# Kernel optimization log

Hardware: AMD Instinct MI355X
Metric: run time of the kernel (lower is better)

## Reference

```python
import jax, jax.numpy as jnp
import numpy as np

N_NODES = 50000
N_EDGES = 800000
D_IN = 256
D_HID = 256
D_OUT = 256


def setup_inputs() -> dict:
    key = jax.random.key(0)
    ks = jax.random.split(key, 14)
    s = 1.0 / np.sqrt(D_IN)
    inp = {
        "x": jax.random.normal(ks[0], (N_NODES, D_IN), dtype=jnp.float32),
        "edge_index": jax.random.randint(ks[1], (2, N_EDGES), 0, N_NODES, dtype=jnp.int64),
        "edge_attr": jax.random.uniform(ks[2], (N_EDGES, 1), dtype=jnp.float32),
        # GCNConv layer weights (3 layers)
        "W1": jax.random.normal(ks[3], (D_IN, D_HID), dtype=jnp.float32) * s,
        "b1": jnp.zeros((D_HID,), dtype=jnp.float32),
        "W2": jax.random.normal(ks[4], (D_HID, D_HID), dtype=jnp.float32) * s,
        "b2": jnp.zeros((D_HID,), dtype=jnp.float32),
        "W3": jax.random.normal(ks[5], (D_HID, D_OUT), dtype=jnp.float32) * s,
        "b3": jnp.zeros((D_OUT,), dtype=jnp.float32),
        # edge MLP: Linear(1,8) -> ReLU -> Linear(8,1) -> Sigmoid
        "mw1": jax.random.normal(ks[6], (1, 8), dtype=jnp.float32),
        "mb1": jnp.zeros((8,), dtype=jnp.float32),
        "mw2": jax.random.normal(ks[7], (8, 1), dtype=jnp.float32) * (1.0 / np.sqrt(8.0)),
        "mb2": jnp.zeros((1,), dtype=jnp.float32),
    }
    return inp


def _gcn_layer(x, src, dst, ew, W, b, n):
    """PyG GCNConv: add self-loops (weight 1), symmetric normalization."""
    deg = jax.ops.segment_sum(ew, dst, num_segments=n) + 1.0  # self-loop contributes 1
    dinv = jax.lax.rsqrt(deg)                                 # [N]
    norm = dinv[src] * ew * dinv[dst]                         # [E]
    h = x @ W + b                                             # [N, d_out]
    agg = jax.ops.segment_sum(h[src] * norm[:, None], dst, num_segments=n)
    # self-loop term: dinv[i] * 1 * dinv[i] = 1/deg[i]
    return agg + h * (1.0 / deg)[:, None]


def reference(x, edge_index, edge_attr, W1, b1, W2, b2, W3, b3, mw1, mb1, mw2, mb2):
    src, dst = edge_index[0], edge_index[1]
    # edge weight MLP with sigmoid gate
    h = jax.nn.relu(edge_attr @ mw1 + mb1)
    ew = jax.nn.sigmoid(h @ mw2 + mb2)[:, 0]  # [E]

    n = x.shape[0]
    x = jax.nn.relu(_gcn_layer(x, src, dst, ew, W1, b1, n))  # dropout inactive (eval)
    x = jax.nn.relu(_gcn_layer(x, src, dst, ew, W2, b2, n))
    x = _gcn_layer(x, src, dst, ew, W3, b3, n)
    return x
```

## Files before the change

### kernel.cpp

```cpp
#include <hip/hip_runtime.h>
#include <hip/hip_bf16.h>
#include <stdint.h>

#define GCN_N 50000
#define GCN_E 800000
#define GCN_D 256

typedef __attribute__((ext_vector_type(8))) short bf16x8;
typedef __attribute__((ext_vector_type(4))) float f32x4;
typedef unsigned short ushort_t;
typedef unsigned long long u64;

__device__ __forceinline__ float bf2f(ushort_t u) {
    return __uint_as_float(((unsigned)u) << 16);
}
__device__ __forceinline__ ushort_t f2bf(float f) {
    unsigned v = __float_as_uint(f);
    v += 0x7FFFu + ((v >> 16) & 1u);
    return (ushort_t)(v >> 16);
}


__global__ void edge_mlp_kernel(const float* __restrict__ attr,
                                const int* __restrict__ dst,
                                const float* __restrict__ mw1, const float* __restrict__ mb1,
                                const float* __restrict__ mw2, const float* __restrict__ mb2,
                                float* __restrict__ ew, u64* __restrict__ dc,
                                int* __restrict__ rank, int e_count) {
    int e = blockIdx.x * blockDim.x + threadIdx.x;
    if (e >= e_count) return;
    float a = attr[e];
    float s = mb2[0];
#pragma unroll
    for (int j = 0; j < 8; ++j) {
        float hj = fmaf(a, mw1[j], mb1[j]);
        hj = fmaxf(hj, 0.0f);
        s = fmaf(hj, mw2[j], s);
    }
    float w = 1.0f / (1.0f + expf(-s));
    ew[e] = w;
    u64 pack = (1ull << 40) + (u64)((double)w * 4294967296.0);
    u64 old = atomicAdd(&dc[dst[e]], pack);
    rank[e] = (int)(old >> 40);
}

__global__ __launch_bounds__(1024) void scan1_kernel(const u64* __restrict__ dc,
                                                     int* __restrict__ part,
                                                     int* __restrict__ bsum,
                                                     float* __restrict__ dinv,
                                                     float* __restrict__ invdeg, int n) {
    __shared__ int s[1024];
    int tid = threadIdx.x;
    int i = blockIdx.x * 1024 + tid;
    u64 dv = (i < n) ? dc[i] : 0ull;
    int v = (int)(dv >> 40);
    s[tid] = v;
    if (i < n) {
        float wsum = (float)((double)(dv & ((1ull << 40) - 1)) * (1.0 / 4294967296.0));
        float d = 1.0f + wsum;
        dinv[i] = rsqrtf(d);
        invdeg[i] = 1.0f / d;
    }
    __syncthreads();
#pragma unroll
    for (int d = 1; d < 1024; d <<= 1) {
        int t = (tid >= d) ? s[tid - d] : 0;
        __syncthreads();
        s[tid] += t;
        __syncthreads();
    }
    if (i < n) part[i] = s[tid] - v;
    if (tid == 1023) bsum[blockIdx.x] = s[1023];
}

__global__ void scan2_kernel(int* bsum, int nb) {
    int t = threadIdx.x;
    int orig = (t < nb) ? bsum[t] : 0;
    int v = orig;
#pragma unroll
    for (int d = 1; d < 64; d <<= 1) {
        int u = __shfl_up(v, d, 64);
        if (t >= d) v += u;
    }
    if (t < nb) bsum[t] = v - orig;
}

__global__ void scan3_kernel(const int* __restrict__ part, const int* __restrict__ bsum,
                             int* __restrict__ offs, int n, int e_total) {
    int i = blockIdx.x * blockDim.x + threadIdx.x;
    if (i < n) offs[i] = part[i] + bsum[i >> 10];
    if (i == 0) offs[n] = e_total;
}

__global__ void scatter_kernel(const int* __restrict__ src, const int* __restrict__ dst,
                               const float* __restrict__ ew, const float* __restrict__ dinv,
                               const int* __restrict__ offs, const int* __restrict__ rank,
                               int2* __restrict__ csr, int e_count) {
    int e = blockIdx.x * blockDim.x + threadIdx.x;
    if (e >= e_count) return;
    int sN = src[e], dN = dst[e];
    int pos = offs[dN] + rank[e];
    float w = dinv[sN] * ew[e] * dinv[dN];
    csr[pos] = make_int2(sN, __float_as_int(w));
}


__global__ __launch_bounds__(256) void wconvert_kernel(
        const float* __restrict__ W1, const float* __restrict__ W2,
        const float* __restrict__ W3,
        ushort_t* __restrict__ wtf) {
    __shared__ ushort_t lds_hi[32][256];
    __shared__ ushort_t lds_lo[32][256];
    const int layer = blockIdx.x >> 3;
    const int kt = blockIdx.x & 7;
    const float* W = (layer == 0) ? W1 : (layer == 1) ? W2 : W3;
    ushort_t* wtf_hi = wtf + (size_t)layer * 2 * 65536;
    ushort_t* wtf_lo = wtf_hi + 65536;
    const int tid = threadIdx.x;
    for (int c = 0; c < 32; ++c) {
        float f = W[(kt * 32 + c) * GCN_D + tid];
        unsigned u = __float_as_uint(f);
        ushort_t hi = (ushort_t)(u >> 16);
        float r = f - __uint_as_float(u & 0xFFFF0000u);
        lds_hi[c][tid] = hi;
        lds_lo[c][tid] = f2bf(r);
    }
    __syncthreads();
#pragma unroll
    for (int q = 0; q < 4; ++q) {
        int slot = q * 256 + tid;
        int lane = slot & 63, nt = slot >> 6;
        int n = nt * 16 + (lane & 15);
        int kl = (lane >> 4) * 8;
        ushort_t h8[8], l8[8];
#pragma unroll
        for (int j = 0; j < 8; ++j) { h8[j] = lds_hi[kl + j][n]; l8[j] = lds_lo[kl + j][n]; }
        size_t o = ((size_t)(kt * 16 + nt) * 64 + lane) * 8;
#pragma unroll
        for (int j = 0; j < 8; ++j) { wtf_hi[o + j] = h8[j]; wtf_lo[o + j] = l8[j]; }
    }
}


__device__ __forceinline__ void split_f32x8(float4 f0, float4 f1, bf16x8& hi, bf16x8& lo) {
    float f[8] = {f0.x, f0.y, f0.z, f0.w, f1.x, f1.y, f1.z, f1.w};
#pragma unroll
    for (int i = 0; i < 8; ++i) {
        unsigned u = __float_as_uint(f[i]);
        hi[i] = (short)(u >> 16);
        float r = f[i] - __uint_as_float(u & 0xFFFF0000u);
        lo[i] = (short)f2bf(r);
    }
}

__global__ __launch_bounds__(256) void mfma_gemm_f32_kernel(
        const float* __restrict__ x,
        const ushort_t* __restrict__ wtf_hi,
        const ushort_t* __restrict__ wtf_lo,
        const float* __restrict__ bias,
        ushort_t* __restrict__ out_h,
        int n_rows) {
    __shared__ ushort_t smem[4 * 16 * 264];
    const int tid  = threadIdx.x;
    const int lane = tid & 63;
    const int wv   = tid >> 6;
    const int r16  = lane & 15;
    const int kg   = lane >> 4;
    const int row0 = blockIdx.x * 64 + wv * 16;

    f32x4 acc[16];
#pragma unroll
    for (int nt = 0; nt < 16; ++nt) acc[nt] = (f32x4){0.f, 0.f, 0.f, 0.f};

    const int arow = row0 + r16;
    const float* ap = (arow < n_rows) ? &x[(size_t)arow * GCN_D + kg * 8] : nullptr;
    bf16x8* sH = (bf16x8*)smem;
    bf16x8* sL = ((bf16x8*)smem) + 1024;

#pragma unroll 1
    for (int kt = 0; kt < 8; ++kt) {
        float4 f0 = make_float4(0.f, 0.f, 0.f, 0.f), f1 = f0;
        if (ap) {
            f0 = *(const float4*)(ap + kt * 32);
            f1 = *(const float4*)(ap + kt * 32 + 4);
        }
        const bf16x8* gh = (const bf16x8*)wtf_hi + (size_t)kt * 1024;
        const bf16x8* gl = (const bf16x8*)wtf_lo + (size_t)kt * 1024;
        bf16x8 t0 = gh[tid], t1 = gh[256 + tid], t2 = gh[512 + tid], t3 = gh[768 + tid];
        bf16x8 u0 = gl[tid], u1 = gl[256 + tid], u2 = gl[512 + tid], u3 = gl[768 + tid];
        sH[tid] = t0; sH[256 + tid] = t1; sH[512 + tid] = t2; sH[768 + tid] = t3;
        sL[tid] = u0; sL[256 + tid] = u1; sL[512 + tid] = u2; sL[768 + tid] = u3;
        bf16x8 a_hi, a_lo;
        split_f32x8(f0, f1, a_hi, a_lo);
        __syncthreads();
#pragma unroll
        for (int nt = 0; nt < 16; ++nt) {
            bf16x8 bh = sH[nt * 64 + lane];
            bf16x8 bl = sL[nt * 64 + lane];
            acc[nt] = __builtin_amdgcn_mfma_f32_16x16x32_bf16(a_hi, bh, acc[nt], 0, 0, 0);
            acc[nt] = __builtin_amdgcn_mfma_f32_16x16x32_bf16(a_lo, bh, acc[nt], 0, 0, 0);
            acc[nt] = __builtin_amdgcn_mfma_f32_16x16x32_bf16(a_hi, bl, acc[nt], 0, 0, 0);
        }
        __syncthreads();
    }

    ushort_t* my = smem + wv * (16 * 264);
#pragma unroll
    for (int nt = 0; nt < 16; ++nt) {
        float bv = bias[nt * 16 + r16];
#pragma unroll
        for (int r = 0; r < 4; ++r)
            my[(kg * 4 + r) * 264 + nt * 16 + r16] = f2bf(acc[nt][r] + bv);
    }
#pragma unroll 4
    for (int r = 0; r < 16; ++r) {
        int row = row0 + r;
        if (row < n_rows) {
            ushort4 v = *(ushort4*)&my[r * 264 + lane * 4];
            *(ushort4*)&out_h[(size_t)row * GCN_D + lane * 4] = v;
        }
    }
}


__global__ __launch_bounds__(256) void mfma_gemm_bf16_kernel(
        const ushort_t* __restrict__ a_in,
        const ushort_t* __restrict__ wtf_hi,
        const float* __restrict__ bias,
        ushort_t* __restrict__ out_h,
        int n_rows) {
    __shared__ ushort_t smem[4 * 16 * 264];
    const int tid  = threadIdx.x;
    const int lane = tid & 63;
    const int wv   = tid >> 6;
    const int r16  = lane & 15;
    const int kg   = lane >> 4;
    const int row0 = blockIdx.x * 64 + wv * 16;

    f32x4 acc[16];
#pragma unroll
    for (int nt = 0; nt < 16; ++nt) acc[nt] = (f32x4){0.f, 0.f, 0.f, 0.f};

    const int arow = row0 + r16;
    const ushort_t* ap = (arow < n_rows) ? &a_in[(size_t)arow * GCN_D + kg * 8] : nullptr;
    bf16x8* sH = (bf16x8*)smem;

#pragma unroll 1
    for (int kp = 0; kp < 4; ++kp) {
        const bf16x8* gh = (const bf16x8*)wtf_hi + (size_t)kp * 2048;
        bf16x8 t[8];
#pragma unroll
        for (int j = 0; j < 8; ++j) t[j] = gh[j * 256 + tid];
        bf16x8 a0 = (bf16x8){0,0,0,0,0,0,0,0}, a1 = a0;
        if (ap) {
            a0 = *(const bf16x8*)(ap + (kp * 2) * 32);
            a1 = *(const bf16x8*)(ap + (kp * 2 + 1) * 32);
        }
#pragma unroll
        for (int j = 0; j < 8; ++j) sH[j * 256 + tid] = t[j];
        __syncthreads();
#pragma unroll
        for (int nt = 0; nt < 16; ++nt) {
            bf16x8 bh0 = sH[nt * 64 + lane];
            bf16x8 bh1 = sH[1024 + nt * 64 + lane];
            acc[nt] = __builtin_amdgcn_mfma_f32_16x16x32_bf16(a0, bh0, acc[nt], 0, 0, 0);
            acc[nt] = __builtin_amdgcn_mfma_f32_16x16x32_bf16(a1, bh1, acc[nt], 0, 0, 0);
        }
        __syncthreads();
    }

    ushort_t* my = smem + wv * (16 * 264);
#pragma unroll
    for (int nt = 0; nt < 16; ++nt) {
        float bv = bias[nt * 16 + r16];
#pragma unroll
        for (int r = 0; r < 4; ++r)
            my[(kg * 4 + r) * 264 + nt * 16 + r16] = f2bf(acc[nt][r] + bv);
    }
#pragma unroll 4
    for (int r = 0; r < 16; ++r) {
        int row = row0 + r;
        if (row < n_rows) {
            ushort4 v = *(ushort4*)&my[r * 264 + lane * 4];
            *(ushort4*)&out_h[(size_t)row * GCN_D + lane * 4] = v;
        }
    }
}


template <int OUT_BF16>
__global__ __launch_bounds__(256) void spmm_kernel(const ushort_t* __restrict__ h,
                                                   const int* __restrict__ offs,
                                                   const int2* __restrict__ csr,
                                                   const float* __restrict__ invdeg,
                                                   void* __restrict__ outp, int n) {
    int wid = (blockIdx.x * blockDim.x + threadIdx.x) >> 6;
    int lane = threadIdx.x & 63;
    if (wid >= n) return;
    const ushort4* h4 = (const ushort4*)h;
    ushort4 sv = h4[(size_t)wid * 64 + lane];
    float sw = invdeg[wid];
    float4 acc;
    acc.x = bf2f(sv.x) * sw; acc.y = bf2f(sv.y) * sw;
    acc.z = bf2f(sv.z) * sw; acc.w = bf2f(sv.w) * sw;
    int e0 = offs[wid], e1 = offs[wid + 1];
    int k = e0;
    for (; k + 8 <= e1; k += 8) {
        int2 ee[8]; ushort4 vv[8];
#pragma unroll
        for (int u = 0; u < 8; ++u) ee[u] = csr[k + u];
#pragma unroll
        for (int u = 0; u < 8; ++u) vv[u] = h4[(size_t)ee[u].x * 64 + lane];
#pragma unroll
        for (int u = 0; u < 8; ++u) {
            float w = __int_as_float(ee[u].y);
            acc.x = fmaf(w, bf2f(vv[u].x), acc.x);
            acc.y = fmaf(w, bf2f(vv[u].y), acc.y);
            acc.z = fmaf(w, bf2f(vv[u].z), acc.z);
            acc.w = fmaf(w, bf2f(vv[u].w), acc.w);
        }
    }
    for (; k < e1; ++k) {
        int2 e = csr[k];
        float w = __int_as_float(e.y);
        ushort4 hv = h4[(size_t)e.x * 64 + lane];
        acc.x = fmaf(w, bf2f(hv.x), acc.x);
        acc.y = fmaf(w, bf2f(hv.y), acc.y);
        acc.z = fmaf(w, bf2f(hv.z), acc.z);
        acc.w = fmaf(w, bf2f(hv.w), acc.w);
    }
    if (OUT_BF16) {
        ushort4 o;
        o.x = f2bf(fmaxf(acc.x, 0.f));
        o.y = f2bf(fmaxf(acc.y, 0.f));
        o.z = f2bf(fmaxf(acc.z, 0.f));
        o.w = f2bf(fmaxf(acc.w, 0.f));
        ((ushort4*)outp)[(size_t)wid * 64 + lane] = o;
    } else {
        ((float4*)outp)[(size_t)wid * 64 + lane] = acc;
    }
}


extern "C" void kernel_launch(void* const* d_in, const int* in_sizes, int n_in,
                              void* d_out, int out_size, void* d_ws, size_t ws_size,
                              hipStream_t stream) {
    const float* x    = (const float*)d_in[0];
    const int*   ei   = (const int*)d_in[1];
    const float* attr = (const float*)d_in[2];
    const float* W1 = (const float*)d_in[3];  const float* b1 = (const float*)d_in[4];
    const float* W2 = (const float*)d_in[5];  const float* b2 = (const float*)d_in[6];
    const float* W3 = (const float*)d_in[7];  const float* b3 = (const float*)d_in[8];
    const float* mw1 = (const float*)d_in[9]; const float* mb1 = (const float*)d_in[10];
    const float* mw2 = (const float*)d_in[11];const float* mb2 = (const float*)d_in[12];
    float* out = (float*)d_out;

    const int N = GCN_N, E = GCN_E;
    const int* srcI = ei;
    const int* dstI = ei + E;

    char* ws = (char*)d_ws;
    float* ew     = (float*)ws;                      ws += (size_t)E * 4;
    int*   rank   = (int*)ws;                        ws += (size_t)E * 4;
    u64*   dc     = (u64*)(((uintptr_t)ws + 255) & ~(uintptr_t)255); ws = (char*)(dc + N);
    float* dinv   = (float*)ws;                      ws += (size_t)N * 4;
    float* invdeg = (float*)ws;                      ws += (size_t)N * 4;
    int*   offs   = (int*)ws;                        ws += (size_t)(N + 1) * 4;
    int*   bsum   = (int*)ws;                        ws += 64 * 4;
    int*   part   = (int*)ws;                        ws += (size_t)N * 4;
    int2*  csr    = (int2*)(((uintptr_t)ws + 255) & ~(uintptr_t)255); ws = (char*)(csr + E);
    ushort_t* h   = (ushort_t*)(((uintptr_t)ws + 255) & ~(uintptr_t)255);
    ws = (char*)(h + (size_t)N * GCN_D);
    ushort_t* act = (ushort_t*)(((uintptr_t)ws + 255) & ~(uintptr_t)255);
    ws = (char*)(act + (size_t)N * GCN_D);
    ushort_t* wtf = (ushort_t*)(((uintptr_t)ws + 255) & ~(uintptr_t)255);
    ushort_t* wtf_hi1 = wtf;
    ushort_t* wtf_lo1 = wtf + 65536;
    ushort_t* wtf_hi2 = wtf + 2 * 65536;
    ushort_t* wtf_hi3 = wtf + 4 * 65536;

    hipMemsetAsync(dc, 0, (size_t)N * sizeof(u64), stream);
    edge_mlp_kernel<<<(E + 255) / 256, 256, 0, stream>>>(attr, dstI, mw1, mb1, mw2, mb2,
                                                         ew, dc, rank, E);
    int nb = (N + 1023) / 1024;
    scan1_kernel<<<nb, 1024, 0, stream>>>(dc, part, bsum, dinv, invdeg, N);
    scan2_kernel<<<1, 64, 0, stream>>>(bsum, nb);
    scan3_kernel<<<(N + 255) / 256, 256, 0, stream>>>(part, bsum, offs, N, E);
    scatter_kernel<<<(E + 255) / 256, 256, 0, stream>>>(srcI, dstI, ew, dinv, offs, rank,
                                                        csr, E);
    wconvert_kernel<<<24, 256, 0, stream>>>(W1, W2, W3, wtf);

    const int gemm_grid = (N + 63) / 64;
    const int spmm_grid = (N * 64 + 255) / 256;

    mfma_gemm_f32_kernel<<<gemm_grid, 256, 0, stream>>>(x, wtf_hi1, wtf_lo1, b1, h, N);
    spmm_kernel<1><<<spmm_grid, 256, 0, stream>>>(h, offs, csr, invdeg, act, N);
    mfma_gemm_bf16_kernel<<<gemm_grid, 256, 0, stream>>>(act, wtf_hi2, b2, h, N);
    spmm_kernel<1><<<spmm_grid, 256, 0, stream>>>(h, offs, csr, invdeg, act, N);
    mfma_gemm_bf16_kernel<<<gemm_grid, 256, 0, stream>>>(act, wtf_hi3, b3, h, N);
    spmm_kernel<0><<<spmm_grid, 256, 0, stream>>>(h, offs, csr, invdeg, out, N);
}
```

Before: 335.2 us.

## Fuse layer-1 GEMM, edge MLP and W2/W3 conversion into one heterogeneous launch

The first-layer GEMM, the edge-weight MLP with its degree/rank atomics, and the W2/W3 weight conversion now run as block ranges of a single kernel. W1 conversion moves into its own small kernel launched beforehand. The aim is to overlap independent work, so the atomic-heavy edge pass fills the GPU alongside the MFMA GEMM, and to cut launch count. In exchange, all blocks carry the GEMM's LDS allocation, which may limit occupancy for the light edge blocks, and the W1 conversion becomes a separate serial step.

```diff
diff --git a/kernel.cpp b/kernel.cpp
--- a/kernel.cpp
+++ b/kernel.cpp
@@ -5,6 +5,9 @@
 #define GCN_N 50000
 #define GCN_E 800000
 #define GCN_D 256
+
+#define GEMM_BLOCKS ((GCN_N + 63) / 64)
+#define EDGE_BLOCKS ((GCN_E + 255) / 256)
 
 typedef __attribute__((ext_vector_type(8))) short bf16x8;
 typedef __attribute__((ext_vector_type(4))) float f32x4;
@@ -20,29 +23,152 @@
     return (ushort_t)(v >> 16);
 }
 
-
-__global__ void edge_mlp_kernel(const float* __restrict__ attr,
-                                const int* __restrict__ dst,
-                                const float* __restrict__ mw1, const float* __restrict__ mb1,
-                                const float* __restrict__ mw2, const float* __restrict__ mb2,
-                                float* __restrict__ ew, u64* __restrict__ dc,
-                                int* __restrict__ rank, int e_count) {
-    int e = blockIdx.x * blockDim.x + threadIdx.x;
-    if (e >= e_count) return;
-    float a = attr[e];
-    float s = mb2[0];
-#pragma unroll
-    for (int j = 0; j < 8; ++j) {
-        float hj = fmaf(a, mw1[j], mb1[j]);
-        hj = fmaxf(hj, 0.0f);
-        s = fmaf(hj, mw2[j], s);
-    }
-    float w = 1.0f / (1.0f + expf(-s));
-    ew[e] = w;
-    u64 pack = (1ull << 40) + (u64)((double)w * 4294967296.0);
-    u64 old = atomicAdd(&dc[dst[e]], pack);
-    rank[e] = (int)(old >> 40);
-}
+__device__ __forceinline__ void split_f32x8(float4 f0, float4 f1, bf16x8& hi, bf16x8& lo) {
+    float f[8] = {f0.x, f0.y, f0.z, f0.w, f1.x, f1.y, f1.z, f1.w};
+#pragma unroll
+    for (int i = 0; i < 8; ++i) {
+        unsigned u = __float_as_uint(f[i]);
+        hi[i] = (short)(u >> 16);
+        float r = f[i] - __uint_as_float(u & 0xFFFF0000u);
+        lo[i] = (short)f2bf(r);
+    }
+}
+
+__device__ __forceinline__ void wconv_body(const float* __restrict__ W, int kt, int tid,
+                                           ushort_t* __restrict__ wtf_hi,
+                                           ushort_t* __restrict__ wtf_lo,
+                                           ushort_t* smem) {
+    ushort_t (*lds_hi)[256] = (ushort_t(*)[256])smem;
+    ushort_t (*lds_lo)[256] = (ushort_t(*)[256])(smem + 8192);
+    for (int c = 0; c < 32; ++c) {
+        float f = W[(kt * 32 + c) * GCN_D + tid];
+        unsigned u = __float_as_uint(f);
+        lds_hi[c][tid] = (ushort_t)(u >> 16);
+        float r = f - __uint_as_float(u & 0xFFFF0000u);
+        lds_lo[c][tid] = f2bf(r);
+    }
+    __syncthreads();
+#pragma unroll
+    for (int q = 0; q < 4; ++q) {
+        int slot = q * 256 + tid;
+        int lane = slot & 63, nt = slot >> 6;
+        int n = nt * 16 + (lane & 15);
+        int kl = (lane >> 4) * 8;
+        ushort_t h8[8], l8[8];
+#pragma unroll
+        for (int j = 0; j < 8; ++j) { h8[j] = lds_hi[kl + j][n]; l8[j] = lds_lo[kl + j][n]; }
+        size_t o = ((size_t)(kt * 16 + nt) * 64 + lane) * 8;
+#pragma unroll
+        for (int j = 0; j < 8; ++j) { wtf_hi[o + j] = h8[j]; wtf_lo[o + j] = l8[j]; }
+    }
+}
+
+__global__ __launch_bounds__(256) void wconv1_kernel(const float* __restrict__ W,
+                                                     ushort_t* __restrict__ wtf) {
+    __shared__ ushort_t smem[16384];
+    wconv_body(W, blockIdx.x, threadIdx.x, wtf, wtf + 65536, smem);
+}
+
+
+__global__ __launch_bounds__(256) void fused1_kernel(
+        const float* __restrict__ x, const ushort_t* __restrict__ wtf_hi1,
+        const ushort_t* __restrict__ wtf_lo1, const float* __restrict__ b1,
+        ushort_t* __restrict__ out_h,
+        const float* __restrict__ attr, const int* __restrict__ dst,
+        const float* __restrict__ mw1, const float* __restrict__ mb1,
+        const float* __restrict__ mw2, const float* __restrict__ mb2,
+        float* __restrict__ ew, u64* __restrict__ dc, int* __restrict__ rank,
+        const float* __restrict__ W2, const float* __restrict__ W3,
+        ushort_t* __restrict__ wtf) {
+    __shared__ ushort_t smem[4 * 16 * 264];
+    const int b = blockIdx.x;
+    const int tid = threadIdx.x;
+
+    if (b < GEMM_BLOCKS) {
+        const int lane = tid & 63;
+        const int wv   = tid >> 6;
+        const int r16  = lane & 15;
+        const int kg   = lane >> 4;
+        const int row0 = b * 64 + wv * 16;
+
+        f32x4 acc[16];
+#pragma unroll
+        for (int nt = 0; nt < 16; ++nt) acc[nt] = (f32x4){0.f, 0.f, 0.f, 0.f};
+
+        const int arow = row0 + r16;
+        const float* ap = (arow < GCN_N) ? &x[(size_t)arow * GCN_D + kg * 8] : nullptr;
+        bf16x8* sH = (bf16x8*)smem;
+        bf16x8* sL = ((bf16x8*)smem) + 1024;
+
+#pragma unroll 1
+        for (int kt = 0; kt < 8; ++kt) {
+            float4 f0 = make_float4(0.f, 0.f, 0.f, 0.f), f1 = f0;
+            if (ap) {
+                f0 = *(const float4*)(ap + kt * 32);
+                f1 = *(const float4*)(ap + kt * 32 + 4);
+            }
+            const bf16x8* gh = (const bf16x8*)wtf_hi1 + (size_t)kt * 1024;
+            const bf16x8* gl = (const bf16x8*)wtf_lo1 + (size_t)kt * 1024;
+            bf16x8 t0 = gh[tid], t1 = gh[256 + tid], t2 = gh[512 + tid], t3 = gh[768 + tid];
+            bf16x8 u0 = gl[tid], u1 = gl[256 + tid], u2 = gl[512 + tid], u3 = gl[768 + tid];
+            sH[tid] = t0; sH[256 + tid] = t1; sH[512 + tid] = t2; sH[768 + tid] = t3;
+            sL[tid] = u0; sL[256 + tid] = u1; sL[512 + tid] = u2; sL[768 + tid] = u3;
+            bf16x8 a_hi, a_lo;
+            split_f32x8(f0, f1, a_hi, a_lo);
+            __syncthreads();
+#pragma unroll
+            for (int nt = 0; nt < 16; ++nt) {
+                bf16x8 bh = sH[nt * 64 + lane];
+                bf16x8 bl = sL[nt * 64 + lane];
+                acc[nt] = __builtin_amdgcn_mfma_f32_16x16x32_bf16(a_hi, bh, acc[nt], 0, 0, 0);
+                acc[nt] = __builtin_amdgcn_mfma_f32_16x16x32_bf16(a_lo, bh, acc[nt], 0, 0, 0);
+                acc[nt] = __builtin_amdgcn_mfma_f32_16x16x32_bf16(a_hi, bl, acc[nt], 0, 0, 0);
+            }
+            __syncthreads();
+        }
+
+        ushort_t* my = smem + wv * (16 * 264);
+#pragma unroll
+        for (int nt = 0; nt < 16; ++nt) {
+            float bv = b1[nt * 16 + r16];
+#pragma unroll
+            for (int r = 0; r < 4; ++r)
+                my[(kg * 4 + r) * 264 + nt * 16 + r16] = f2bf(acc[nt][r] + bv);
+        }
+#pragma unroll 4
+        for (int r = 0; r < 16; ++r) {
+            int row = row0 + r;
+            if (row < GCN_N) {
+                ushort4 v = *(ushort4*)&my[r * 264 + lane * 4];
+                *(ushort4*)&out_h[(size_t)row * GCN_D + lane * 4] = v;
+            }
+        }
+    } else if (b < GEMM_BLOCKS + EDGE_BLOCKS) {
+        int e = (b - GEMM_BLOCKS) * 256 + tid;
+        if (e >= GCN_E) return;
+        float a = attr[e];
+        float s = mb2[0];
+#pragma unroll
+        for (int j = 0; j < 8; ++j) {
+            float hj = fmaf(a, mw1[j], mb1[j]);
+            hj = fmaxf(hj, 0.0f);
+            s = fmaf(hj, mw2[j], s);
+        }
+        float w = 1.0f / (1.0f + expf(-s));
+        ew[e] = w;
+        u64 pack = (1ull << 40) + (u64)((double)w * 4294967296.0);
+        u64 old = atomicAdd(&dc[dst[e]], pack);
+        rank[e] = (int)(old >> 40);
+    } else {
+        const int wb = b - GEMM_BLOCKS - EDGE_BLOCKS;
+        const int layer = 1 + (wb >> 3);
+        const int kt = wb & 7;
+        const float* W = (layer == 1) ? W2 : W3;
+        ushort_t* wtf_hi = wtf + (size_t)layer * 2 * 65536;
+        wconv_body(W, kt, tid, wtf_hi, wtf_hi + 65536, smem);
+    }
+}
+
 
 __global__ __launch_bounds__(1024) void scan1_kernel(const u64* __restrict__ dc,
                                                      int* __restrict__ part,
@@ -102,124 +228,6 @@
     int pos = offs[dN] + rank[e];
     float w = dinv[sN] * ew[e] * dinv[dN];
     csr[pos] = make_int2(sN, __float_as_int(w));
-}
-
-
-__global__ __launch_bounds__(256) void wconvert_kernel(
-        const float* __restrict__ W1, const float* __restrict__ W2,
-        const float* __restrict__ W3,
-        ushort_t* __restrict__ wtf) {
-    __shared__ ushort_t lds_hi[32][256];
-    __shared__ ushort_t lds_lo[32][256];
-    const int layer = blockIdx.x >> 3;
-    const int kt = blockIdx.x & 7;
-    const float* W = (layer == 0) ? W1 : (layer == 1) ? W2 : W3;
-    ushort_t* wtf_hi = wtf + (size_t)layer * 2 * 65536;
-    ushort_t* wtf_lo = wtf_hi + 65536;
-    const int tid = threadIdx.x;
-    for (int c = 0; c < 32; ++c) {
-        float f = W[(kt * 32 + c) * GCN_D + tid];
-        unsigned u = __float_as_uint(f);
-        ushort_t hi = (ushort_t)(u >> 16);
-        float r = f - __uint_as_float(u & 0xFFFF0000u);
-        lds_hi[c][tid] = hi;
-        lds_lo[c][tid] = f2bf(r);
-    }
-    __syncthreads();
-#pragma unroll
-    for (int q = 0; q < 4; ++q) {
-        int slot = q * 256 + tid;
-        int lane = slot & 63, nt = slot >> 6;
-        int n = nt * 16 + (lane & 15);
-        int kl = (lane >> 4) * 8;
-        ushort_t h8[8], l8[8];
-#pragma unroll
-        for (int j = 0; j < 8; ++j) { h8[j] = lds_hi[kl + j][n]; l8[j] = lds_lo[kl + j][n]; }
-        size_t o = ((size_t)(kt * 16 + nt) * 64 + lane) * 8;
-#pragma unroll
-        for (int j = 0; j < 8; ++j) { wtf_hi[o + j] = h8[j]; wtf_lo[o + j] = l8[j]; }
-    }
-}
-
-
-__device__ __forceinline__ void split_f32x8(float4 f0, float4 f1, bf16x8& hi, bf16x8& lo) {
-    float f[8] = {f0.x, f0.y, f0.z, f0.w, f1.x, f1.y, f1.z, f1.w};
-#pragma unroll
-    for (int i = 0; i < 8; ++i) {
-        unsigned u = __float_as_uint(f[i]);
-        hi[i] = (short)(u >> 16);
-        float r = f[i] - __uint_as_float(u & 0xFFFF0000u);
-        lo[i] = (short)f2bf(r);
-    }
-}
-
-__global__ __launch_bounds__(256) void mfma_gemm_f32_kernel(
-        const float* __restrict__ x,
-        const ushort_t* __restrict__ wtf_hi,
-        const ushort_t* __restrict__ wtf_lo,
-        const float* __restrict__ bias,
-        ushort_t* __restrict__ out_h,
-        int n_rows) {
-    __shared__ ushort_t smem[4 * 16 * 264];
-    const int tid  = threadIdx.x;
-    const int lane = tid & 63;
-    const int wv   = tid >> 6;
-    const int r16  = lane & 15;
-    const int kg   = lane >> 4;
-    const int row0 = blockIdx.x * 64 + wv * 16;
-
-    f32x4 acc[16];
-#pragma unroll
-    for (int nt = 0; nt < 16; ++nt) acc[nt] = (f32x4){0.f, 0.f, 0.f, 0.f};
-
-    const int arow = row0 + r16;
-    const float* ap = (arow < n_rows) ? &x[(size_t)arow * GCN_D + kg * 8] : nullptr;
-    bf16x8* sH = (bf16x8*)smem;
-    bf16x8* sL = ((bf16x8*)smem) + 1024;
-
-#pragma unroll 1
-    for (int kt = 0; kt < 8; ++kt) {
-        float4 f0 = make_float4(0.f, 0.f, 0.f, 0.f), f1 = f0;
-        if (ap) {
-            f0 = *(const float4*)(ap + kt * 32);
-            f1 = *(const float4*)(ap + kt * 32 + 4);
-        }
-        const bf16x8* gh = (const bf16x8*)wtf_hi + (size_t)kt * 1024;
-        const bf16x8* gl = (const bf16x8*)wtf_lo + (size_t)kt * 1024;
-        bf16x8 t0 = gh[tid], t1 = gh[256 + tid], t2 = gh[512 + tid], t3 = gh[768 + tid];
-        bf16x8 u0 = gl[tid], u1 = gl[256 + tid], u2 = gl[512 + tid], u3 = gl[768 + tid];
-        sH[tid] = t0; sH[256 + tid] = t1; sH[512 + tid] = t2; sH[768 + tid] = t3;
-        sL[tid] = u0; sL[256 + tid] = u1; sL[512 + tid] = u2; sL[768 + tid] = u3;
-        bf16x8 a_hi, a_lo;
-        split_f32x8(f0, f1, a_hi, a_lo);
-        __syncthreads();
-#pragma unroll
-        for (int nt = 0; nt < 16; ++nt) {
-            bf16x8 bh = sH[nt * 64 + lane];
-            bf16x8 bl = sL[nt * 64 + lane];
-            acc[nt] = __builtin_amdgcn_mfma_f32_16x16x32_bf16(a_hi, bh, acc[nt], 0, 0, 0);
-            acc[nt] = __builtin_amdgcn_mfma_f32_16x16x32_bf16(a_lo, bh, acc[nt], 0, 0, 0);
-            acc[nt] = __builtin_amdgcn_mfma_f32_16x16x32_bf16(a_hi, bl, acc[nt], 0, 0, 0);
-        }
-        __syncthreads();
-    }
-
-    ushort_t* my = smem + wv * (16 * 264);
-#pragma unroll
-    for (int nt = 0; nt < 16; ++nt) {
-        float bv = bias[nt * 16 + r16];
-#pragma unroll
-        for (int r = 0; r < 4; ++r)
-            my[(kg * 4 + r) * 264 + nt * 16 + r16] = f2bf(acc[nt][r] + bv);
-    }
-#pragma unroll 4
-    for (int r = 0; r < 16; ++r) {
-        int row = row0 + r;
-        if (row < n_rows) {
-            ushort4 v = *(ushort4*)&my[r * 264 + lane * 4];
-            *(ushort4*)&out_h[(size_t)row * GCN_D + lane * 4] = v;
-        }
-    }
 }
 
 
@@ -380,20 +388,21 @@
     ushort_t* wtf_hi3 = wtf + 4 * 65536;
 
     hipMemsetAsync(dc, 0, (size_t)N * sizeof(u64), stream);
-    edge_mlp_kernel<<<(E + 255) / 256, 256, 0, stream>>>(attr, dstI, mw1, mb1, mw2, mb2,
-                                                         ew, dc, rank, E);
+    wconv1_kernel<<<8, 256, 0, stream>>>(W1, wtf);
+    fused1_kernel<<<GEMM_BLOCKS + EDGE_BLOCKS + 16, 256, 0, stream>>>(
+        x, wtf_hi1, wtf_lo1, b1, h,
+        attr, dstI, mw1, mb1, mw2, mb2, ew, dc, rank,
+        W2, W3, wtf);
     int nb = (N + 1023) / 1024;
     scan1_kernel<<<nb, 1024, 0, stream>>>(dc, part, bsum, dinv, invdeg, N);
     scan2_kernel<<<1, 64, 0, stream>>>(bsum, nb);
     scan3_kernel<<<(N + 255) / 256, 256, 0, stream>>>(part, bsum, offs, N, E);
     scatter_kernel<<<(E + 255) / 256, 256, 0, stream>>>(srcI, dstI, ew, dinv, offs, rank,
                                                         csr, E);
-    wconvert_kernel<<<24, 256, 0, stream>>>(W1, W2, W3, wtf);
 
     const int gemm_grid = (N + 63) / 64;
     const int spmm_grid = (N * 64 + 255) / 256;
 
-    mfma_gemm_f32_kernel<<<gemm_grid, 256, 0, stream>>>(x, wtf_hi1, wtf_lo1, b1, h, N);
     spmm_kernel<1><<<spmm_grid, 256, 0, stream>>>(h, offs, csr, invdeg, act, N);
     mfma_gemm_bf16_kernel<<<gemm_grid, 256, 0, stream>>>(act, wtf_hi2, b2, h, N);
     spmm_kernel<1><<<spmm_grid, 256, 0, stream>>>(h, offs, csr, invdeg, act, N);
```

New measurement: 326.8 us. -2.5%, faster.
